# Kernel tuning notes

Measured on AMD Instinct MI355X. Metric: run time of the kernel, lower is better.

Reference implementation:

```python
import jax, jax.numpy as jnp
import numpy as np

KERNEL_SIZE = 10
CHANNELS = 3
MEAN = (KERNEL_SIZE - 1) // 2  # 4


def setup_inputs() -> dict:
    key = jax.random.key(0)
    x = jax.random.uniform(key, (32, CHANNELS, 512, 512), dtype=jnp.float32)
    return {"x": x}


def reference(x) -> jnp.ndarray:
    # (1 - x) * 0.5, then replicate pad by MEAN on H and W
    y = (1.0 - x) * 0.5
    y = jnp.pad(y, ((0, 0), (0, 0), (MEAN, MEAN), (MEAN, MEAN)), mode="edge")
    # depthwise (groups=channels) conv with all-ones 10x10 kernel, VALID padding
    # weight layout OIHW with O=CHANNELS, I=1 (feature_group_count=CHANNELS)
    w = jnp.ones((CHANNELS, 1, KERNEL_SIZE, KERNEL_SIZE), dtype=x.dtype)
    out = jax.lax.conv_general_dilated(
        y, w,
        window_strides=(1, 1),
        padding="VALID",
        dimension_numbers=("NCHW", "OIHW", "NCHW"),
        feature_group_count=CHANNELS,
    )
    return out  # [B, C, H-1, W-1]
```

## Files before the change

### kernel.cpp

```cpp
#include <hip/hip_runtime.h>


#define IMG 512
#define OUTW 511
#define KS 10
#define MEAN 4
#define SUB 32
#define TSTREAM (SUB + KS - 1)

__global__ __launch_bounds__(256) void onedilate_kernel(
    const float* __restrict__ x, float* __restrict__ out)
{
    const int tid = threadIdx.x;
    const int j   = tid & 127;
    const int sub = tid >> 7;
    const int rb  = blockIdx.x * 64 + sub * SUB;
    const int bc  = blockIdx.y;

    const float* __restrict__ xim = x + (size_t)bc * IMG * IMG;
    float* __restrict__ oim = out + (size_t)bc * OUTW * OUTW;

    const int b0  = 4 * j - 4;
    const int bl0 = max(b0, 0);
    const int b2  = 4 * j + 4;
    const int bl2 = min(b2, IMG - 4);
    const bool lo0 = (b0 < 0);
    const bool hi2 = (b2 > IMG - 4);
    const int c12 = min(4 * j + 8, IMG - 1);

    float4 ring[KS];
    #pragma unroll
    for (int k = 0; k < KS; ++k) ring[k] = make_float4(0.f, 0.f, 0.f, 0.f);
    float4 V = make_float4(0.f, 0.f, 0.f, 0.f);

    const int cbase = 4 * j;

    for (int t0 = 0; t0 < TSTREAM; t0 += KS) {
        #pragma unroll
        for (int u = 0; u < KS; ++u) {
            int s = t0 + u;
            if (s < TSTREAM) {
                int ri = min(max(rb + s - MEAN, 0), IMG - 1);
                const float* __restrict__ rowp = xim + ri * IMG;

                float4 v0 = *(const float4*)(rowp + bl0);
                float4 v1 = *(const float4*)(rowp + cbase);
                float4 v2 = *(const float4*)(rowp + bl2);
                float w12 = rowp[c12];
                if (lo0) v0 = make_float4(v0.x, v0.x, v0.x, v0.x);
                if (hi2) v2 = make_float4(v2.w, v2.w, v2.w, v2.w);

                float S = v0.x + v0.y + v0.z + v0.w
                        + v1.x + v1.y + v1.z + v1.w
                        + v2.x + v2.y;
                float4 H;
                H.x = S;
                S += v2.z - v0.x; H.y = S;
                S += v2.w - v0.y; H.z = S;
                S += w12  - v0.z; H.w = S;

                V.x += H.x - ring[u].x;
                V.y += H.y - ring[u].y;
                V.z += H.z - ring[u].z;
                V.w += H.w - ring[u].w;
                ring[u] = H;

                if (s >= KS - 1) {
                    int i = rb + s - (KS - 1);
                    if (i < OUTW) {
                        float* op = oim + (size_t)i * OUTW + cbase;
                        op[0] = 50.0f - 0.5f * V.x;
                        op[1] = 50.0f - 0.5f * V.y;
                        op[2] = 50.0f - 0.5f * V.z;
                        if (cbase + 3 < OUTW) op[3] = 50.0f - 0.5f * V.w;
                    }
                }
            }
        }
    }
}

extern "C" void kernel_launch(void* const* d_in, const int* in_sizes, int n_in,
                              void* d_out, int out_size, void* d_ws, size_t ws_size,
                              hipStream_t stream) {
    const float* x = (const float*)d_in[0];
    float* out = (float*)d_out;

    dim3 block(256, 1, 1);
    dim3 grid(IMG / 64,
              32 * 3,
              1);
    onedilate_kernel<<<grid, block, 0, stream>>>(x, out);
}
```

Before: 190.5 us.

## Halve rows per thread, fully unroll stream, and prefetch next row

Each thread now streams 16 output rows instead of 32, which doubles the grid in the row dimension. The row loop is fully unrolled with register prefetch of the next input row, so load latency overlaps with the current row's sums. The ring zero-init is dropped in favour of a conditional subtract. The cost is more redundant halo reads: 25 input rows are read per 16 outputs instead of 41 per 32.

```diff
diff --git a/kernel.cpp b/kernel.cpp
--- a/kernel.cpp
+++ b/kernel.cpp
@@ -5,8 +5,9 @@
 #define OUTW 511
 #define KS 10
 #define MEAN 4
-#define SUB 32
-#define TSTREAM (SUB + KS - 1)
+#define ROWS 32
+#define SUBROWS 16
+#define TSTREAM (SUBROWS + KS - 1)
 
 __global__ __launch_bounds__(256) void onedilate_kernel(
     const float* __restrict__ x, float* __restrict__ out)
@@ -14,7 +15,7 @@
     const int tid = threadIdx.x;
     const int j   = tid & 127;
     const int sub = tid >> 7;
-    const int rb  = blockIdx.x * 64 + sub * SUB;
+    const int rb  = blockIdx.x * ROWS + sub * SUBROWS;
     const int bc  = blockIdx.y;
 
     const float* __restrict__ xim = x + (size_t)bc * IMG * IMG;
@@ -27,55 +28,62 @@
     const bool lo0 = (b0 < 0);
     const bool hi2 = (b2 > IMG - 4);
     const int c12 = min(4 * j + 8, IMG - 1);
+    const int cbase = 4 * j;
 
     float4 ring[KS];
-    #pragma unroll
-    for (int k = 0; k < KS; ++k) ring[k] = make_float4(0.f, 0.f, 0.f, 0.f);
     float4 V = make_float4(0.f, 0.f, 0.f, 0.f);
 
-    const int cbase = 4 * j;
+    {
+        const int ri0 = min(max(rb - MEAN, 0), IMG - 1);
+        const float* rp = xim + ri0 * IMG;
+        float4 c0 = *(const float4*)(rp + bl0);
+        float4 c1 = *(const float4*)(rp + cbase);
+        float4 c2 = *(const float4*)(rp + bl2);
+        float cw  = rp[c12];
 
-    for (int t0 = 0; t0 < TSTREAM; t0 += KS) {
         #pragma unroll
-        for (int u = 0; u < KS; ++u) {
-            int s = t0 + u;
-            if (s < TSTREAM) {
-                int ri = min(max(rb + s - MEAN, 0), IMG - 1);
-                const float* __restrict__ rowp = xim + ri * IMG;
+        for (int s = 0; s < TSTREAM; ++s) {
+            float4 n0, n1, n2; float nw;
+            if (s + 1 < TSTREAM) {
+                int ri = min(max(rb + s + 1 - MEAN, 0), IMG - 1);
+                const float* np = xim + ri * IMG;
+                n0 = *(const float4*)(np + bl0);
+                n1 = *(const float4*)(np + cbase);
+                n2 = *(const float4*)(np + bl2);
+                nw = np[c12];
+            }
 
-                float4 v0 = *(const float4*)(rowp + bl0);
-                float4 v1 = *(const float4*)(rowp + cbase);
-                float4 v2 = *(const float4*)(rowp + bl2);
-                float w12 = rowp[c12];
-                if (lo0) v0 = make_float4(v0.x, v0.x, v0.x, v0.x);
-                if (hi2) v2 = make_float4(v2.w, v2.w, v2.w, v2.w);
+            float4 a0 = c0, a2 = c2;
+            if (lo0) a0 = make_float4(c0.x, c0.x, c0.x, c0.x);
+            if (hi2) a2 = make_float4(c2.w, c2.w, c2.w, c2.w);
+            float S = a0.x + a0.y + a0.z + a0.w
+                    + c1.x + c1.y + c1.z + c1.w
+                    + a2.x + a2.y;
+            float4 H;
+            H.x = S;
+            S += a2.z - a0.x; H.y = S;
+            S += a2.w - a0.y; H.z = S;
+            S += cw  - a0.z;  H.w = S;
 
-                float S = v0.x + v0.y + v0.z + v0.w
-                        + v1.x + v1.y + v1.z + v1.w
-                        + v2.x + v2.y;
-                float4 H;
-                H.x = S;
-                S += v2.z - v0.x; H.y = S;
-                S += v2.w - v0.y; H.z = S;
-                S += w12  - v0.z; H.w = S;
+            if (s >= KS) {
+                const float4 old = ring[s % KS];
+                V.x -= old.x; V.y -= old.y; V.z -= old.z; V.w -= old.w;
+            }
+            V.x += H.x; V.y += H.y; V.z += H.z; V.w += H.w;
+            ring[s % KS] = H;
 
-                V.x += H.x - ring[u].x;
-                V.y += H.y - ring[u].y;
-                V.z += H.z - ring[u].z;
-                V.w += H.w - ring[u].w;
-                ring[u] = H;
-
-                if (s >= KS - 1) {
-                    int i = rb + s - (KS - 1);
-                    if (i < OUTW) {
-                        float* op = oim + (size_t)i * OUTW + cbase;
-                        op[0] = 50.0f - 0.5f * V.x;
-                        op[1] = 50.0f - 0.5f * V.y;
-                        op[2] = 50.0f - 0.5f * V.z;
-                        if (cbase + 3 < OUTW) op[3] = 50.0f - 0.5f * V.w;
-                    }
+            if (s >= KS - 1) {
+                int i = rb + s - (KS - 1);
+                if (i < OUTW) {
+                    float* op = oim + (size_t)i * OUTW + cbase;
+                    op[0] = 50.0f - 0.5f * V.x;
+                    op[1] = 50.0f - 0.5f * V.y;
+                    op[2] = 50.0f - 0.5f * V.z;
+                    if (cbase + 3 < OUTW) op[3] = 50.0f - 0.5f * V.w;
                 }
             }
+
+            if (s + 1 < TSTREAM) { c0 = n0; c1 = n1; c2 = n2; cw = nw; }
         }
     }
 }
@@ -87,7 +95,7 @@
     float* out = (float*)d_out;
 
     dim3 block(256, 1, 1);
-    dim3 grid(IMG / 64,
+    dim3 grid((OUTW + ROWS - 1) / ROWS,
               32 * 3,
               1);
     onedilate_kernel<<<grid, block, 0, stream>>>(x, out);
```

Result: no change. 190.9 us (+0.3%).
